# Optimization experiments

Measured on AMD Instinct MI355X. Metric: run time of the kernel, lower is better.

## Reference

```python
import jax, jax.numpy as jnp
import numpy as np

SCALE = 1.0
P0 = 0.1


def setup_inputs() -> dict:
    key = jax.random.key(0)
    k1, k2, k3, k4 = jax.random.split(key, 4)
    B, N, D, T, TM = 64, 2048, 128, 512, 512
    data = jax.random.normal(k1, (B, N, D), dtype=jnp.float32)
    targets = jax.random.normal(k2, (B, N), dtype=jnp.float32)
    W = jax.random.normal(k3, (D, T), dtype=jnp.float32)        # major task pool, (n_dims, n_tasks)
    W_minor = jax.random.normal(k4, (D, TM), dtype=jnp.float32)  # minor task pool
    return {"data": data, "targets": targets, "W": W, "W_minor": W_minor}


def reference(data, targets, W, W_minor):
    # data: (B, N, D); targets: (B, N); W: (D, T); W_minor: (D, TM)
    n_minor = W_minor.shape[1]
    W_all = jnp.concatenate([W, W_minor], axis=1)            # (D, T_total)
    XW = jnp.einsum('bnd,dt->bnt', data, W_all)              # (B, N, T_total)
    diff2 = (targets[..., None] - XW) ** 2                   # (B, N, T_total)
    # Prefix sum-of-squared-residuals: step i uses points 0..i-1 (step 0 -> zeros,
    # matching the original's zeros-prefix call).
    prefix = jnp.cumsum(diff2, axis=1)
    prefix = jnp.concatenate([jnp.zeros_like(prefix[:, :1]), prefix[:, :-1]], axis=1)
    # Log priors: original hardcodes log((1-p0)/3) for major tasks (kept faithfully).
    log_prior_major = float(np.log((1.0 - P0) / 3.0))
    log_prior_minor = float(np.log(P0 / n_minor))
    log_prior = jnp.concatenate([
        jnp.full((W.shape[1],), log_prior_major, dtype=data.dtype),
        jnp.full((n_minor,), log_prior_minor, dtype=data.dtype),
    ])                                                        # (T_total,)
    log_probs = -0.5 * prefix / (SCALE ** 2) + log_prior      # (B, N, T_total)
    weights = jax.nn.softmax(log_probs, axis=-1)              # posterior over tasks
    w_mmse = jnp.einsum('bnt,dt->bnd', weights, W_all)        # (B, N, D)
    preds = jnp.sum(data * w_mmse, axis=-1)                   # (B, N)
    return preds
```

## Files before the change

kernel.cpp:

```cpp
#include <hip/hip_runtime.h>

typedef _Float16 half8 __attribute__((ext_vector_type(8)));
typedef float floatx4 __attribute__((ext_vector_type(4)));

#define NB 64
#define NN 2048
#define ND 128
#define NT 1024
#define NC 16
#define NCHUNKS 128
#define NIV 64

#define ALPHA 0.84932184f
#define INV_ALPHA 1.17741002f
#define LP2_MAJOR (-1.7369655941662063f)
#define LP2_MINOR (-12.321928094887362f)

__device__ __forceinline__ float fexp2(float x) {
  float r;
  asm("v_exp_f32 %0, %1" : "=v"(r) : "v"(x));
  return r;
}

#define PIN8(x) asm volatile("" : "+v"(x))

template <int CTRL>
__device__ __forceinline__ float dppshr_add(float x) {
  int i = __builtin_bit_cast(int, x);
  int s = __builtin_amdgcn_update_dpp(0, i, CTRL, 0xF, 0xF, true);
  return x + __builtin_bit_cast(float, s);
}
__device__ __forceinline__ float scan16(float x) {
  x = dppshr_add<0x111>(x);
  x = dppshr_add<0x112>(x);
  x = dppshr_add<0x114>(x);
  x = dppshr_add<0x118>(x);
  return x;
}
__device__ __forceinline__ float bcast15(float x) {
  int i = __builtin_bit_cast(int, x);
  i = __builtin_amdgcn_ds_swizzle(i, 0x1F0);
  return __builtin_bit_cast(float, i);
}

__global__ void k_prep(const float* __restrict__ W, const float* __restrict__ Wm,
                       _Float16* __restrict__ Wph, _Float16* __restrict__ Wpl) {
  int idx = blockIdx.x * 256 + threadIdx.x;
  int t = idx >> 7, d = idx & 127;
  float x = (t < 512) ? W[d * 512 + t] : Wm[d * 512 + (t - 512)];
  x *= ALPHA;
  _Float16 h = (_Float16)x;
  _Float16 l = (_Float16)(x - (float)h);
  Wph[idx] = h;
  Wpl[idx] = l;
}

__global__ void k_prep_data(const float* __restrict__ data,
                            _Float16* __restrict__ Apk) {
  int idx = blockIdx.x * 256 + threadIdx.x;
  int l = idx & 63, kk = (idx >> 6) & 3, ch = (idx >> 8) & 127, b = idx >> 15;
  int row = ch * 16 + (l & 15);
  int dcol = kk * 32 + (l >> 4) * 8;
  const float* src = data + ((size_t)b * NN + row) * ND + dcol;
  floatx4 a0 = *(const floatx4*)src;
  floatx4 a1 = *(const floatx4*)(src + 4);
  half8 h, lo;
#pragma unroll
  for (int j = 0; j < 4; ++j) {
    h[j] = (_Float16)a0[j];
    lo[j] = (_Float16)(a0[j] - (float)h[j]);
    h[4 + j] = (_Float16)a1[j];
    lo[4 + j] = (_Float16)(a1[j] - (float)h[4 + j]);
  }
  size_t o = ((size_t)(b * 128 + ch)) * 4096 + kk * 512 + l * 8;
  *(half8*)(Apk + o) = h;
  *(half8*)(Apk + o + 2048) = lo;
}

__global__ __launch_bounds__(256, 2)
void k_fused(const _Float16* __restrict__ Apk, const float* __restrict__ targets,
             const _Float16* __restrict__ Wph, const _Float16* __restrict__ Wpl,
             floatx4* __restrict__ part) {
  int bid = blockIdx.x;
  int xcd = bid & 7, rest = bid >> 3;
  int tq = rest & 7, b = (rest >> 3) * 8 + xcd;
  int tid = threadIdx.x;
  int w = tid >> 6, l = tid & 63;
  int l15 = l & 15, lhi = l >> 4;
  int wavebase = tq * 128 + w * 32;

  half8 wh[2][4], wl[2][4];
#pragma unroll
  for (int tt = 0; tt < 2; ++tt)
#pragma unroll
    for (int kk = 0; kk < 4; ++kk) {
      int off = (wavebase + tt * 16 + l15) * 128 + kk * 32 + lhi * 8;
      wh[tt][kk] = *(const half8*)(Wph + off);
      wl[tt][kk] = *(const half8*)(Wpl + off);
    }
#pragma unroll
  for (int tt = 0; tt < 2; ++tt)
#pragma unroll
    for (int kk = 0; kk < 4; ++kk) { PIN8(wh[tt][kk]); PIN8(wl[tt][kk]); }

  float prior2 = (tq < 4) ? LP2_MAJOR : LP2_MINOR;
  float run[2][4] = {{0.f, 0.f, 0.f, 0.f}, {0.f, 0.f, 0.f, 0.f}};

  const _Float16* abase = Apk + (size_t)b * 128 * 4096;
  const float* tgp = targets + (size_t)b * NN + l15;
  size_t pbase = (size_t)b * NN * 8 + tq;

  __shared__ _Float16 Abuf[2][8192];
  __shared__ float sm[4][4][65][3];

  int t8 = tid * 8;

#define GEMM3(ACC, TT, AH, AL)                                                      \
  do {                                                                              \
    floatx4 hh = {0.f, 0.f, 0.f, 0.f};                                              \
    floatx4 hl = {0.f, 0.f, 0.f, 0.f};                                              \
    floatx4 lh = {0.f, 0.f, 0.f, 0.f};                                              \
    _Pragma("unroll")                                                               \
    for (int kk = 0; kk < 4; ++kk) {                                                \
      hh = __builtin_amdgcn_mfma_f32_16x16x32_f16(wh[TT][kk], AH[kk], hh, 0, 0, 0); \
      hl = __builtin_amdgcn_mfma_f32_16x16x32_f16(wh[TT][kk], AL[kk], hl, 0, 0, 0); \
      lh = __builtin_amdgcn_mfma_f32_16x16x32_f16(wl[TT][kk], AH[kk], lh, 0, 0, 0); \
    }                                                                               \
    ACC = (hh + hl) + lh;                                                           \
  } while (0)

#define EPI(ACC0, ACC1, SLOT, TGOFF)                                  \
  do {                                                                \
    float tgs = tgp[TGOFF] * ALPHA;                                   \
    float q[2][4], inc[2][4], lp[2][4];                               \
    _Pragma("unroll")                                                 \
    for (int r = 0; r < 4; ++r) {                                     \
      float d0 = tgs - ACC0[r], d1 = tgs - ACC1[r];                   \
      q[0][r] = d0 * d0; q[1][r] = d1 * d1;                           \
    }                                                                 \
    _Pragma("unroll")                                                 \
    for (int tt = 0; tt < 2; ++tt)                                    \
      _Pragma("unroll")                                               \
      for (int r = 0; r < 4; ++r) inc[tt][r] = scan16(q[tt][r]);      \
    _Pragma("unroll")                                                 \
    for (int tt = 0; tt < 2; ++tt)                                    \
      _Pragma("unroll")                                               \
      for (int r = 0; r < 4; ++r) {                                   \
        lp[tt][r] = (prior2 - run[tt][r]) + (q[tt][r] - inc[tt][r]);  \
        run[tt][r] += bcast15(inc[tt][r]);                            \
      }                                                               \
    float m = fmaxf(fmaxf(fmaxf(lp[0][0], lp[0][1]),                  \
                          fmaxf(lp[0][2], lp[0][3])),                 \
                    fmaxf(fmaxf(lp[1][0], lp[1][1]),                  \
                          fmaxf(lp[1][2], lp[1][3])));                \
    float s1 = 0.f, s2 = 0.f;                                         \
    _Pragma("unroll")                                                 \
    for (int r = 0; r < 4; ++r) {                                     \
      float e0 = fexp2(lp[0][r] - m), e1 = fexp2(lp[1][r] - m);       \
      s1 += e0 + e1;                                                  \
      s2 = fmaf(e0, ACC0[r], s2);                                     \
      s2 = fmaf(e1, ACC1[r], s2);                                     \
    }                                                                 \
    sm[w][SLOT][l][0] = m;                                            \
    sm[w][SLOT][l][1] = s1;                                           \
    sm[w][SLOT][l][2] = s2;                                           \
  } while (0)

  half8 s0 = *(const half8*)(abase + t8);
  half8 s1_ = *(const half8*)(abase + 2048 + t8);
  half8 s2_ = *(const half8*)(abase + 4096 + t8);
  half8 s3 = *(const half8*)(abase + 6144 + t8);
  *(half8*)&Abuf[0][t8] = s0;
  *(half8*)&Abuf[0][2048 + t8] = s1_;
  *(half8*)&Abuf[0][4096 + t8] = s2_;
  *(half8*)&Abuf[0][6144 + t8] = s3;
  s0 = *(const half8*)(abase + 8192 + t8);
  s1_ = *(const half8*)(abase + 8192 + 2048 + t8);
  s2_ = *(const half8*)(abase + 8192 + 4096 + t8);
  s3 = *(const half8*)(abase + 8192 + 6144 + t8);
  __syncthreads();

  for (int iv = 0; iv < NIV; ++iv) {
    int cur = iv & 1;
    half8 ah[4], al[4];
#pragma unroll
    for (int kk = 0; kk < 4; ++kk) {
      ah[kk] = *(const half8*)&Abuf[cur][kk * 512 + l * 8];
      al[kk] = *(const half8*)&Abuf[cur][2048 + kk * 512 + l * 8];
    }
    floatx4 accA0, accA1;
    GEMM3(accA0, 0, ah, al);
    GEMM3(accA1, 1, ah, al);
#pragma unroll
    for (int kk = 0; kk < 4; ++kk) {
      ah[kk] = *(const half8*)&Abuf[cur][4096 + kk * 512 + l * 8];
      al[kk] = *(const half8*)&Abuf[cur][6144 + kk * 512 + l * 8];
    }
    floatx4 accB0, accB1;
    GEMM3(accB0, 0, ah, al);
    GEMM3(accB1, 1, ah, al);

    *(half8*)&Abuf[cur ^ 1][t8] = s0;
    *(half8*)&Abuf[cur ^ 1][2048 + t8] = s1_;
    *(half8*)&Abuf[cur ^ 1][4096 + t8] = s2_;
    *(half8*)&Abuf[cur ^ 1][6144 + t8] = s3;
    {
      int pf = iv + 2 > 63 ? 63 : iv + 2;
      const _Float16* pp = abase + (size_t)pf * 8192 + t8;
      s0 = *(const half8*)pp;
      s1_ = *(const half8*)(pp + 2048);
      s2_ = *(const half8*)(pp + 4096);
      s3 = *(const half8*)(pp + 6144);
    }

    EPI(accA0, accA1, ((2 * iv) & 3), 0);
    EPI(accB0, accB1, ((2 * iv + 1) & 3), 16);

    if (iv & 1) {
      __syncthreads();
      if (tid < 64) {
        int c4 = tid >> 4, row = tid & 15;
        float M = -3.4e38f;
#pragma unroll
        for (int wv = 0; wv < 4; ++wv)
#pragma unroll
          for (int g = 0; g < 4; ++g)
            M = fmaxf(M, sm[wv][c4][g * 16 + row][0]);
        float S1 = 0.f, S2 = 0.f;
#pragma unroll
        for (int wv = 0; wv < 4; ++wv)
#pragma unroll
          for (int g = 0; g < 4; ++g) {
            float e = fexp2(sm[wv][c4][g * 16 + row][0] - M);
            S1 = fmaf(sm[wv][c4][g * 16 + row][1], e, S1);
            S2 = fmaf(sm[wv][c4][g * 16 + row][2], e, S2);
          }
        floatx4 v;
        v[0] = M; v[1] = S1; v[2] = S2; v[3] = 0.f;
        part[pbase + (size_t)((2 * iv - 2 + c4) * 16 + row) * 8] = v;
      }
    }
    __syncthreads();
    tgp += 32;
  }
#undef EPI
#undef GEMM3
}

__global__ void k_combine(const floatx4* __restrict__ part, float* __restrict__ out) {
  int idx = blockIdx.x * 256 + threadIdx.x;
  const floatx4* p = part + (size_t)idx * 8;
  floatx4 v[8];
  float M = -3.4e38f;
#pragma unroll
  for (int j = 0; j < 8; ++j) { v[j] = p[j]; M = fmaxf(M, v[j][0]); }
  float s1 = 0.f, s2 = 0.f;
#pragma unroll
  for (int j = 0; j < 8; ++j) {
    float e = fexp2(v[j][0] - M);
    s1 += v[j][1] * e;
    s2 += v[j][2] * e;
  }
  out[idx] = s2 / s1 * INV_ALPHA;
}

extern "C" void kernel_launch(void* const* d_in, const int* in_sizes, int n_in,
                              void* d_out, int out_size, void* d_ws, size_t ws_size,
                              hipStream_t stream) {
  const float* data    = (const float*)d_in[0];
  const float* targets = (const float*)d_in[1];
  const float* W       = (const float*)d_in[2];
  const float* Wm      = (const float*)d_in[3];
  float* out = (float*)d_out;

  char* ws = (char*)d_ws;
  const size_t MB = 1u << 20;
  _Float16* Wph  = (_Float16*)ws;
  _Float16* Wpl  = (_Float16*)(ws + 256 * 1024);
  _Float16* Apk  = (_Float16*)(ws + 512 * 1024);
  floatx4* part  = (floatx4*)(ws + 512 * 1024 + 64 * MB);

  k_prep<<<512, 256, 0, stream>>>(W, Wm, Wph, Wpl);
  k_prep_data<<<8192, 256, 0, stream>>>(data, Apk);
  k_fused<<<NB * 8, 256, 0, stream>>>(Apk, targets, Wph, Wpl, part);
  k_combine<<<(NB * NN) / 256, 256, 0, stream>>>(part, out);
}
```

Before: 176.8 us.

## Software-pipeline GEMM and softmax epilogue across iterations, vectorize epilogue and LDS stores

Restructures the main loop so that each iteration's MFMA GEMM runs alongside the epilogue (scan, softmax partials) of the previous iteration's accumulators, with a peeled prologue and a final drain step. The epilogue is rewritten on floatx4 vectors, folds the prior and the running prefix into a single accumulator, and writes partials to LDS as one 16-byte store. The aim is to let the MFMA and VALU/cross-lane work overlap and to cut scalar instruction count. The cost is extra live accumulators (register pressure) and more involved bookkeeping for the merge slots.

Measured after the change: 177.8 us. Within noise of the previous version (+0.6%).

```diff
diff --git a/kernel.cpp b/kernel.cpp
--- a/kernel.cpp
+++ b/kernel.cpp
@@ -104,14 +104,15 @@
     for (int kk = 0; kk < 4; ++kk) { PIN8(wh[tt][kk]); PIN8(wl[tt][kk]); }
 
   float prior2 = (tq < 4) ? LP2_MAJOR : LP2_MINOR;
-  float run[2][4] = {{0.f, 0.f, 0.f, 0.f}, {0.f, 0.f, 0.f, 0.f}};
+  floatx4 pmr0 = {prior2, prior2, prior2, prior2};
+  floatx4 pmr1 = pmr0;
 
   const _Float16* abase = Apk + (size_t)b * 128 * 4096;
   const float* tgp = targets + (size_t)b * NN + l15;
   size_t pbase = (size_t)b * NN * 8 + tq;
 
   __shared__ _Float16 Abuf[2][8192];
-  __shared__ float sm[4][4][65][3];
+  __shared__ floatx4 sm4[4][4][65];
 
   int t8 = tid * 8;
 
@@ -129,42 +130,71 @@
     ACC = (hh + hl) + lh;                                                           \
   } while (0)
 
-#define EPI(ACC0, ACC1, SLOT, TGOFF)                                  \
+#define EPI(A0, A1, SLOT, TGS)                                        \
   do {                                                                \
-    float tgs = tgp[TGOFF] * ALPHA;                                   \
-    float q[2][4], inc[2][4], lp[2][4];                               \
+    floatx4 tg4 = {(TGS), (TGS), (TGS), (TGS)};                       \
+    floatx4 d0 = tg4 - (A0), d1 = tg4 - (A1);                         \
+    floatx4 q0 = d0 * d0, q1 = d1 * d1;                               \
+    floatx4 i0, i1;                                                   \
     _Pragma("unroll")                                                 \
     for (int r = 0; r < 4; ++r) {                                     \
-      float d0 = tgs - ACC0[r], d1 = tgs - ACC1[r];                   \
-      q[0][r] = d0 * d0; q[1][r] = d1 * d1;                           \
+      i0[r] = scan16(q0[r]); i1[r] = scan16(q1[r]);                   \
     }                                                                 \
-    _Pragma("unroll")                                                 \
-    for (int tt = 0; tt < 2; ++tt)                                    \
-      _Pragma("unroll")                                               \
-      for (int r = 0; r < 4; ++r) inc[tt][r] = scan16(q[tt][r]);      \
-    _Pragma("unroll")                                                 \
-    for (int tt = 0; tt < 2; ++tt)                                    \
-      _Pragma("unroll")                                               \
-      for (int r = 0; r < 4; ++r) {                                   \
-        lp[tt][r] = (prior2 - run[tt][r]) + (q[tt][r] - inc[tt][r]);  \
-        run[tt][r] += bcast15(inc[tt][r]);                            \
-      }                                                               \
-    float m = fmaxf(fmaxf(fmaxf(lp[0][0], lp[0][1]),                  \
-                          fmaxf(lp[0][2], lp[0][3])),                 \
-                    fmaxf(fmaxf(lp[1][0], lp[1][1]),                  \
-                          fmaxf(lp[1][2], lp[1][3])));                \
-    float s1 = 0.f, s2 = 0.f;                                         \
+    floatx4 lp0 = pmr0 + (q0 - i0);                                   \
+    floatx4 lp1 = pmr1 + (q1 - i1);                                   \
     _Pragma("unroll")                                                 \
     for (int r = 0; r < 4; ++r) {                                     \
-      float e0 = fexp2(lp[0][r] - m), e1 = fexp2(lp[1][r] - m);       \
-      s1 += e0 + e1;                                                  \
-      s2 = fmaf(e0, ACC0[r], s2);                                     \
-      s2 = fmaf(e1, ACC1[r], s2);                                     \
+      pmr0[r] -= bcast15(i0[r]); pmr1[r] -= bcast15(i1[r]);           \
     }                                                                 \
-    sm[w][SLOT][l][0] = m;                                            \
-    sm[w][SLOT][l][1] = s1;                                           \
-    sm[w][SLOT][l][2] = s2;                                           \
+    float m = fmaxf(fmaxf(fmaxf(lp0[0], lp0[1]), fmaxf(lp0[2], lp0[3])), \
+                    fmaxf(fmaxf(lp1[0], lp1[1]), fmaxf(lp1[2], lp1[3]))); \
+    floatx4 m4 = {m, m, m, m};                                        \
+    floatx4 x0 = lp0 - m4, x1 = lp1 - m4;                             \
+    floatx4 e0, e1;                                                   \
+    _Pragma("unroll")                                                 \
+    for (int r = 0; r < 4; ++r) { e0[r] = fexp2(x0[r]); e1[r] = fexp2(x1[r]); } \
+    floatx4 s1v = e0 + e1;                                            \
+    floatx4 s2v = e0 * (A0) + e1 * (A1);                              \
+    floatx4 outv;                                                     \
+    outv[0] = m;                                                      \
+    outv[1] = (s1v[0] + s1v[1]) + (s1v[2] + s1v[3]);                  \
+    outv[2] = (s2v[0] + s2v[1]) + (s2v[2] + s2v[3]);                  \
+    outv[3] = 0.f;                                                    \
+    sm4[w][SLOT][l] = outv;                                           \
   } while (0)
+
+#define MERGE(BASECH)                                                 \
+  do {                                                                \
+    if (tid < 64) {                                                   \
+      int c4 = tid >> 4, row = tid & 15;                              \
+      float M = -3.4e38f;                                             \
+      _Pragma("unroll")                                               \
+      for (int wv = 0; wv < 4; ++wv)                                  \
+        _Pragma("unroll")                                             \
+        for (int g = 0; g < 4; ++g)                                   \
+          M = fmaxf(M, sm4[wv][c4][g * 16 + row][0]);                 \
+      float S1 = 0.f, S2 = 0.f;                                       \
+      _Pragma("unroll")                                               \
+      for (int wv = 0; wv < 4; ++wv)                                  \
+        _Pragma("unroll")                                             \
+        for (int g = 0; g < 4; ++g) {                                 \
+          floatx4 vv = sm4[wv][c4][g * 16 + row];                     \
+          float e = fexp2(vv[0] - M);                                 \
+          S1 = fmaf(vv[1], e, S1);                                    \
+          S2 = fmaf(vv[2], e, S2);                                    \
+        }                                                             \
+      floatx4 v;                                                      \
+      v[0] = M; v[1] = S1; v[2] = S2; v[3] = 0.f;                     \
+      part[pbase + (size_t)(((BASECH) + c4) * 16 + row) * 8] = v;     \
+    }                                                                 \
+  } while (0)
+
+#define LOADFRAGS(OFF)                                                \
+  _Pragma("unroll")                                                   \
+  for (int kk = 0; kk < 4; ++kk) {                                    \
+    ah[kk] = *(const half8*)&Abuf[cur][(OFF) + kk * 512 + l * 8];     \
+    al[kk] = *(const half8*)&Abuf[cur][(OFF) + 2048 + kk * 512 + l * 8]; \
+  }
 
   half8 s0 = *(const half8*)(abase + t8);
   half8 s1_ = *(const half8*)(abase + 2048 + t8);
@@ -180,25 +210,45 @@
   s3 = *(const half8*)(abase + 8192 + 6144 + t8);
   __syncthreads();
 
-  for (int iv = 0; iv < NIV; ++iv) {
+  floatx4 pA0, pA1, pB0, pB1;
+  float ptgA, ptgB;
+
+  {
+    int cur = 0;
+    half8 ah[4], al[4];
+    LOADFRAGS(0);
+    GEMM3(pA0, 0, ah, al);
+    GEMM3(pA1, 1, ah, al);
+    LOADFRAGS(4096);
+    GEMM3(pB0, 0, ah, al);
+    GEMM3(pB1, 1, ah, al);
+    ptgA = tgp[0] * ALPHA;
+    ptgB = tgp[16] * ALPHA;
+    *(half8*)&Abuf[1][t8] = s0;
+    *(half8*)&Abuf[1][2048 + t8] = s1_;
+    *(half8*)&Abuf[1][4096 + t8] = s2_;
+    *(half8*)&Abuf[1][6144 + t8] = s3;
+    const _Float16* pp = abase + 2 * 8192 + t8;
+    s0 = *(const half8*)pp;
+    s1_ = *(const half8*)(pp + 2048);
+    s2_ = *(const half8*)(pp + 4096);
+    s3 = *(const half8*)(pp + 6144);
+    __syncthreads();
+    tgp += 32;
+  }
+
+  for (int iv = 1; iv < NIV; ++iv) {
     int cur = iv & 1;
     half8 ah[4], al[4];
-#pragma unroll
-    for (int kk = 0; kk < 4; ++kk) {
-      ah[kk] = *(const half8*)&Abuf[cur][kk * 512 + l * 8];
-      al[kk] = *(const half8*)&Abuf[cur][2048 + kk * 512 + l * 8];
-    }
-    floatx4 accA0, accA1;
-    GEMM3(accA0, 0, ah, al);
-    GEMM3(accA1, 1, ah, al);
-#pragma unroll
-    for (int kk = 0; kk < 4; ++kk) {
-      ah[kk] = *(const half8*)&Abuf[cur][4096 + kk * 512 + l * 8];
-      al[kk] = *(const half8*)&Abuf[cur][6144 + kk * 512 + l * 8];
-    }
-    floatx4 accB0, accB1;
-    GEMM3(accB0, 0, ah, al);
-    GEMM3(accB1, 1, ah, al);
+    floatx4 aA0, aA1, aB0, aB1;
+    LOADFRAGS(0);
+    GEMM3(aA0, 0, ah, al);
+    GEMM3(aA1, 1, ah, al);
+    LOADFRAGS(4096);
+    GEMM3(aB0, 0, ah, al);
+    GEMM3(aB1, 1, ah, al);
+    float tgA = tgp[0] * ALPHA;
+    float tgB = tgp[16] * ALPHA;
 
     *(half8*)&Abuf[cur ^ 1][t8] = s0;
     *(half8*)&Abuf[cur ^ 1][2048 + t8] = s1_;
@@ -213,38 +263,29 @@
       s3 = *(const half8*)(pp + 6144);
     }
 
-    EPI(accA0, accA1, ((2 * iv) & 3), 0);
-    EPI(accB0, accB1, ((2 * iv + 1) & 3), 16);
-
-    if (iv & 1) {
+    EPI(pA0, pA1, ((2 * iv - 2) & 3), ptgA);
+    EPI(pB0, pB1, ((2 * iv - 1) & 3), ptgB);
+
+    if (!(iv & 1)) {
       __syncthreads();
-      if (tid < 64) {
-        int c4 = tid >> 4, row = tid & 15;
-        float M = -3.4e38f;
-#pragma unroll
-        for (int wv = 0; wv < 4; ++wv)
-#pragma unroll
-          for (int g = 0; g < 4; ++g)
-            M = fmaxf(M, sm[wv][c4][g * 16 + row][0]);
-        float S1 = 0.f, S2 = 0.f;
-#pragma unroll
-        for (int wv = 0; wv < 4; ++wv)
-#pragma unroll
-          for (int g = 0; g < 4; ++g) {
-            float e = fexp2(sm[wv][c4][g * 16 + row][0] - M);
-            S1 = fmaf(sm[wv][c4][g * 16 + row][1], e, S1);
-            S2 = fmaf(sm[wv][c4][g * 16 + row][2], e, S2);
-          }
-        floatx4 v;
-        v[0] = M; v[1] = S1; v[2] = S2; v[3] = 0.f;
-        part[pbase + (size_t)((2 * iv - 2 + c4) * 16 + row) * 8] = v;
-      }
+      MERGE(2 * iv - 4);
     }
     __syncthreads();
+
+    pA0 = aA0; pA1 = aA1; pB0 = aB0; pB1 = aB1;
+    ptgA = tgA; ptgB = tgB;
     tgp += 32;
   }
+
+  EPI(pA0, pA1, 2, ptgA);
+  EPI(pB0, pB1, 3, ptgB);
+  __syncthreads();
+  MERGE(124);
+
 #undef EPI
 #undef GEMM3
+#undef MERGE
+#undef LOADFRAGS
 }
 
 __global__ void k_combine(const floatx4* __restrict__ part, float* __restrict__ out) {
```

## Store data low residual as scaled FP8 and use FP8 MFMA for correction term

Applied to the files above, without the earlier changes.

The low-order residual of each data element is scaled by 2^16 and packed as FP8 instead of FP16, and W gets an FP8 copy. The A-low × W-high correction product now runs as an fp8×fp8 MFMA. The W-low × A-high product is kept in FP16 and summed into the second accumulator. This cuts the packed data footprint from 16 to 12 bytes per element pair, reducing global and LDS traffic and the loop's LDS reads. The cost is a coarser correction term, which could reduce accuracy.

After: 168.9 us. 4.4% less time.

```diff
diff --git a/kernel.cpp b/kernel.cpp
--- a/kernel.cpp
+++ b/kernel.cpp
@@ -10,11 +10,15 @@
 #define NC 16
 #define NCHUNKS 128
 #define NIV 64
+#define CHB 6144
+#define IVB 12288
 
 #define ALPHA 0.84932184f
 #define INV_ALPHA 1.17741002f
 #define LP2_MAJOR (-1.7369655941662063f)
 #define LP2_MINOR (-12.321928094887362f)
+#define AL_SCALE 65536.0f
+#define AL_UNSCALE 0x1p-16f
 
 __device__ __forceinline__ float fexp2(float x) {
   float r;
@@ -44,7 +48,8 @@
 }
 
 __global__ void k_prep(const float* __restrict__ W, const float* __restrict__ Wm,
-                       _Float16* __restrict__ Wph, _Float16* __restrict__ Wpl) {
+                       _Float16* __restrict__ Wph, _Float16* __restrict__ Wpl,
+                       unsigned char* __restrict__ Wp8) {
   int idx = blockIdx.x * 256 + threadIdx.x;
   int t = idx >> 7, d = idx & 127;
   float x = (t < 512) ? W[d * 512 + t] : Wm[d * 512 + (t - 512)];
@@ -53,10 +58,12 @@
   _Float16 l = (_Float16)(x - (float)h);
   Wph[idx] = h;
   Wpl[idx] = l;
+  int pk = __builtin_amdgcn_cvt_pk_fp8_f32(x, x, 0, false);
+  Wp8[idx] = (unsigned char)(pk & 0xff);
 }
 
 __global__ void k_prep_data(const float* __restrict__ data,
-                            _Float16* __restrict__ Apk) {
+                            char* __restrict__ Apk) {
   int idx = blockIdx.x * 256 + threadIdx.x;
   int l = idx & 63, kk = (idx >> 6) & 3, ch = (idx >> 8) & 127, b = idx >> 15;
   int row = ch * 16 + (l & 15);
@@ -64,22 +71,29 @@
   const float* src = data + ((size_t)b * NN + row) * ND + dcol;
   floatx4 a0 = *(const floatx4*)src;
   floatx4 a1 = *(const floatx4*)(src + 4);
-  half8 h, lo;
+  half8 h;
+  float alf[8];
 #pragma unroll
   for (int j = 0; j < 4; ++j) {
     h[j] = (_Float16)a0[j];
-    lo[j] = (_Float16)(a0[j] - (float)h[j]);
+    alf[j] = (a0[j] - (float)h[j]) * AL_SCALE;
     h[4 + j] = (_Float16)a1[j];
-    lo[4 + j] = (_Float16)(a1[j] - (float)h[4 + j]);
+    alf[4 + j] = (a1[j] - (float)h[4 + j]) * AL_SCALE;
   }
-  size_t o = ((size_t)(b * 128 + ch)) * 4096 + kk * 512 + l * 8;
-  *(half8*)(Apk + o) = h;
-  *(half8*)(Apk + o + 2048) = lo;
+  int w0 = __builtin_amdgcn_cvt_pk_fp8_f32(alf[0], alf[1], 0, false);
+  w0 = __builtin_amdgcn_cvt_pk_fp8_f32(alf[2], alf[3], w0, true);
+  int w1 = __builtin_amdgcn_cvt_pk_fp8_f32(alf[4], alf[5], 0, false);
+  w1 = __builtin_amdgcn_cvt_pk_fp8_f32(alf[6], alf[7], w1, true);
+  size_t cb = (size_t)(b * 128 + ch) * CHB;
+  *(half8*)(Apk + cb + kk * 1024 + l * 16) = h;
+  int2 pk2 = {w0, w1};
+  *(int2*)(Apk + cb + 4096 + kk * 512 + l * 8) = pk2;
 }
 
 __global__ __launch_bounds__(256, 2)
-void k_fused(const _Float16* __restrict__ Apk, const float* __restrict__ targets,
+void k_fused(const char* __restrict__ Apk, const float* __restrict__ targets,
              const _Float16* __restrict__ Wph, const _Float16* __restrict__ Wpl,
+             const unsigned char* __restrict__ Wp8,
              floatx4* __restrict__ part) {
   int bid = blockIdx.x;
   int xcd = bid & 7, rest = bid >> 3;
@@ -90,6 +104,7 @@
   int wavebase = tq * 128 + w * 32;
 
   half8 wh[2][4], wl[2][4];
+  long w8q[2][4];
 #pragma unroll
   for (int tt = 0; tt < 2; ++tt)
 #pragma unroll
@@ -97,36 +112,40 @@
       int off = (wavebase + tt * 16 + l15) * 128 + kk * 32 + lhi * 8;
       wh[tt][kk] = *(const half8*)(Wph + off);
       wl[tt][kk] = *(const half8*)(Wpl + off);
+      w8q[tt][kk] = *(const long*)(Wp8 + off);
     }
 #pragma unroll
   for (int tt = 0; tt < 2; ++tt)
 #pragma unroll
-    for (int kk = 0; kk < 4; ++kk) { PIN8(wh[tt][kk]); PIN8(wl[tt][kk]); }
+    for (int kk = 0; kk < 4; ++kk) {
+      PIN8(wh[tt][kk]); PIN8(wl[tt][kk]); PIN8(w8q[tt][kk]);
+    }
 
   float prior2 = (tq < 4) ? LP2_MAJOR : LP2_MINOR;
   float run[2][4] = {{0.f, 0.f, 0.f, 0.f}, {0.f, 0.f, 0.f, 0.f}};
 
-  const _Float16* abase = Apk + (size_t)b * 128 * 4096;
+  const char* abase = Apk + (size_t)b * 128 * CHB;
   const float* tgp = targets + (size_t)b * NN + l15;
   size_t pbase = (size_t)b * NN * 8 + tq;
 
-  __shared__ _Float16 Abuf[2][8192];
+  __shared__ char Abuf[2][IVB];
   __shared__ float sm[4][4][65][3];
 
-  int t8 = tid * 8;
-
-#define GEMM3(ACC, TT, AH, AL)                                                      \
+  int t16 = tid * 16;
+
+#define GEMM3(ACC, TT, AH, A8)                                                      \
   do {                                                                              \
     floatx4 hh = {0.f, 0.f, 0.f, 0.f};                                              \
     floatx4 hl = {0.f, 0.f, 0.f, 0.f};                                              \
-    floatx4 lh = {0.f, 0.f, 0.f, 0.f};                                              \
+    floatx4 l8 = {0.f, 0.f, 0.f, 0.f};                                              \
     _Pragma("unroll")                                                               \
     for (int kk = 0; kk < 4; ++kk) {                                                \
       hh = __builtin_amdgcn_mfma_f32_16x16x32_f16(wh[TT][kk], AH[kk], hh, 0, 0, 0); \
-      hl = __builtin_amdgcn_mfma_f32_16x16x32_f16(wh[TT][kk], AL[kk], hl, 0, 0, 0); \
-      lh = __builtin_amdgcn_mfma_f32_16x16x32_f16(wl[TT][kk], AH[kk], lh, 0, 0, 0); \
+      hl = __builtin_amdgcn_mfma_f32_16x16x32_f16(wl[TT][kk], AH[kk], hl, 0, 0, 0); \
+      l8 = __builtin_amdgcn_mfma_f32_16x16x32_fp8_fp8(w8q[TT][kk], A8[kk], l8, 0, 0, 0); \
     }                                                                               \
-    ACC = (hh + hl) + lh;                                                           \
+    ACC = (hh + hl);                                                                \
+    ACC += l8 * AL_UNSCALE;                                                         \
   } while (0)
 
 #define EPI(ACC0, ACC1, SLOT, TGOFF)                                  \
@@ -166,51 +185,46 @@
     sm[w][SLOT][l][2] = s2;                                           \
   } while (0)
 
-  half8 s0 = *(const half8*)(abase + t8);
-  half8 s1_ = *(const half8*)(abase + 2048 + t8);
-  half8 s2_ = *(const half8*)(abase + 4096 + t8);
-  half8 s3 = *(const half8*)(abase + 6144 + t8);
-  *(half8*)&Abuf[0][t8] = s0;
-  *(half8*)&Abuf[0][2048 + t8] = s1_;
-  *(half8*)&Abuf[0][4096 + t8] = s2_;
-  *(half8*)&Abuf[0][6144 + t8] = s3;
-  s0 = *(const half8*)(abase + 8192 + t8);
-  s1_ = *(const half8*)(abase + 8192 + 2048 + t8);
-  s2_ = *(const half8*)(abase + 8192 + 4096 + t8);
-  s3 = *(const half8*)(abase + 8192 + 6144 + t8);
+#define LOADFRAGS(C)                                                  \
+  _Pragma("unroll")                                                   \
+  for (int kk = 0; kk < 4; ++kk) {                                    \
+    ah[kk] = *(const half8*)&Abuf[cur][(C) * CHB + kk * 1024 + l * 16];        \
+    a8[kk] = *(const long*)&Abuf[cur][(C) * CHB + 4096 + kk * 512 + l * 8];    \
+  }
+
+  half8 s0 = *(const half8*)(abase + t16);
+  half8 s1_ = *(const half8*)(abase + 4096 + t16);
+  half8 s2_ = *(const half8*)(abase + 8192 + t16);
+  *(half8*)&Abuf[0][t16] = s0;
+  *(half8*)&Abuf[0][4096 + t16] = s1_;
+  *(half8*)&Abuf[0][8192 + t16] = s2_;
+  s0 = *(const half8*)(abase + IVB + t16);
+  s1_ = *(const half8*)(abase + IVB + 4096 + t16);
+  s2_ = *(const half8*)(abase + IVB + 8192 + t16);
   __syncthreads();
 
   for (int iv = 0; iv < NIV; ++iv) {
     int cur = iv & 1;
-    half8 ah[4], al[4];
-#pragma unroll
-    for (int kk = 0; kk < 4; ++kk) {
-      ah[kk] = *(const half8*)&Abuf[cur][kk * 512 + l * 8];
-      al[kk] = *(const half8*)&Abuf[cur][2048 + kk * 512 + l * 8];
-    }
+    half8 ah[4];
+    long a8[4];
+    LOADFRAGS(0);
     floatx4 accA0, accA1;
-    GEMM3(accA0, 0, ah, al);
-    GEMM3(accA1, 1, ah, al);
-#pragma unroll
-    for (int kk = 0; kk < 4; ++kk) {
-      ah[kk] = *(const half8*)&Abuf[cur][4096 + kk * 512 + l * 8];
-      al[kk] = *(const half8*)&Abuf[cur][6144 + kk * 512 + l * 8];
-    }
+    GEMM3(accA0, 0, ah, a8);
+    GEMM3(accA1, 1, ah, a8);
+    LOADFRAGS(1);
     floatx4 accB0, accB1;
-    GEMM3(accB0, 0, ah, al);
-    GEMM3(accB1, 1, ah, al);
-
-    *(half8*)&Abuf[cur ^ 1][t8] = s0;
-    *(half8*)&Abuf[cur ^ 1][2048 + t8] = s1_;
-    *(half8*)&Abuf[cur ^ 1][4096 + t8] = s2_;
-    *(half8*)&Abuf[cur ^ 1][6144 + t8] = s3;
+    GEMM3(accB0, 0, ah, a8);
+    GEMM3(accB1, 1, ah, a8);
+
+    *(half8*)&Abuf[cur ^ 1][t16] = s0;
+    *(half8*)&Abuf[cur ^ 1][4096 + t16] = s1_;
+    *(half8*)&Abuf[cur ^ 1][8192 + t16] = s2_;
     {
       int pf = iv + 2 > 63 ? 63 : iv + 2;
-      const _Float16* pp = abase + (size_t)pf * 8192 + t8;
+      const char* pp = abase + (size_t)pf * IVB + t16;
       s0 = *(const half8*)pp;
-      s1_ = *(const half8*)(pp + 2048);
-      s2_ = *(const half8*)(pp + 4096);
-      s3 = *(const half8*)(pp + 6144);
+      s1_ = *(const half8*)(pp + 4096);
+      s2_ = *(const half8*)(pp + 8192);
     }
 
     EPI(accA0, accA1, ((2 * iv) & 3), 0);
@@ -245,6 +259,7 @@
   }
 #undef EPI
 #undef GEMM3
+#undef LOADFRAGS
 }
 
 __global__ void k_combine(const floatx4* __restrict__ part, float* __restrict__ out) {
@@ -275,13 +290,14 @@
 
   char* ws = (char*)d_ws;
   const size_t MB = 1u << 20;
-  _Float16* Wph  = (_Float16*)ws;
-  _Float16* Wpl  = (_Float16*)(ws + 256 * 1024);
-  _Float16* Apk  = (_Float16*)(ws + 512 * 1024);
-  floatx4* part  = (floatx4*)(ws + 512 * 1024 + 64 * MB);
-
-  k_prep<<<512, 256, 0, stream>>>(W, Wm, Wph, Wpl);
+  _Float16* Wph      = (_Float16*)ws;
+  _Float16* Wpl      = (_Float16*)(ws + 256 * 1024);
+  unsigned char* Wp8 = (unsigned char*)(ws + 512 * 1024);
+  char* Apk          = (char*)(ws + 1 * MB);
+  floatx4* part      = (floatx4*)(ws + 49 * MB);
+
+  k_prep<<<512, 256, 0, stream>>>(W, Wm, Wph, Wpl, Wp8);
   k_prep_data<<<8192, 256, 0, stream>>>(data, Apk);
-  k_fused<<<NB * 8, 256, 0, stream>>>(Apk, targets, Wph, Wpl, part);
+  k_fused<<<NB * 8, 256, 0, stream>>>(Apk, targets, Wph, Wpl, Wp8, part);
   k_combine<<<(NB * NN) / 256, 256, 0, stream>>>(part, out);
 }
```
